# Kernel tuning notes

Hardware: AMD Instinct MI355X
Metric: run time of the kernel (lower is better)

Reference implementation:

```python
import jax, jax.numpy as jnp
import numpy as np
from jax import lax

DN = ('NCHW', 'OIHW', 'NCHW')

def conv2d(x, k):
    return lax.conv_general_dilated(x, k, (1, 1), 'SAME', dimension_numbers=DN)

def maxpool(x, k):
    # F.max_pool2d pads with -inf (stride 1, odd k -> SAME)
    return lax.reduce_window(x, jnp.array(-jnp.inf, x.dtype), lax.max,
                             (1, 1, k, k), (1, 1, 1, 1), 'SAME')

def avgpool(x, k):
    # F.avg_pool2d default count_include_pad=True -> sum with zero pad / k*k
    s = lax.reduce_window(x, jnp.array(0.0, x.dtype), lax.add,
                          (1, 1, k, k), (1, 1, 1, 1), 'SAME')
    return s / (k * k)

def erode(x, k):
    return -maxpool(-x, k)

def opening(x, k):
    return maxpool(erode(x, k), k)

def quantile(x, q):
    B = x.shape[0]
    return jnp.quantile(x.reshape(B, -1), q, axis=1).reshape(B, 1, 1, 1).astype(x.dtype)

_SOBEL_X = jnp.array([[-1, 0, 1], [-2, 0, 2], [-1, 0, 1]], jnp.float32).reshape(1, 1, 3, 3)
_SOBEL_Y = jnp.array([[1, 2, 1], [0, 0, 0], [-1, -2, -1]], jnp.float32).reshape(1, 1, 3, 3)

def sobelxy(x):
    return jnp.abs(conv2d(x, _SOBEL_X)) + jnp.abs(conv2d(x, _SOBEL_Y))

def _gauss_window(size=11, sigma=1.5):
    g = np.exp(-((np.arange(size) - size // 2) ** 2) / (2.0 * sigma ** 2))
    g = g / g.sum()
    return jnp.asarray(np.outer(g, g), jnp.float32).reshape(1, 1, size, size)

_SSIM_W = _gauss_window()

def ssim(x, y):
    # standard single-channel SSIM, gaussian 11x11 sigma=1.5, SAME padding
    C1, C2 = 0.01 ** 2, 0.03 ** 2
    mu1, mu2 = conv2d(x, _SSIM_W), conv2d(y, _SSIM_W)
    mu1_sq, mu2_sq, mu12 = mu1 * mu1, mu2 * mu2, mu1 * mu2
    s1 = conv2d(x * x, _SSIM_W) - mu1_sq
    s2 = conv2d(y * y, _SSIM_W) - mu2_sq
    s12 = conv2d(x * y, _SSIM_W) - mu12
    m = ((2 * mu12 + C1) * (2 * s12 + C2)) / ((mu1_sq + mu2_sq + C1) * (s1 + s2 + C2))
    return m.mean()

def compute_saliency(ir1):
    # multi-scale morphological top-hat, max over scales, mean-normalized
    sals = [ir1 - opening(ir1, k) for k in (9, 15, 31)]
    sal = jnp.maximum(jnp.maximum(sals[0], sals[1]), sals[2])
    return sal / (sal.mean(axis=(2, 3), keepdims=True) + 1e-6)

def halo_mask_builder(ir1, vis1):
    # surrogate for undefined PhysicsConsistentHaloMask: halo ring around IR highlights
    bright = (ir1 > quantile(ir1, 0.97)).astype(ir1.dtype)
    dilated = maxpool(bright, 15)
    return jnp.clip(dilated - bright, 0.0, 1.0)

_NEAR_RADIUS = 50
_c = np.arange(-_NEAR_RADIUS, _NEAR_RADIUS + 1)
_yy, _xx = np.meshgrid(_c, _c, indexing='ij')
_DISK = jnp.asarray((( _xx * _xx + _yy * _yy) <= _NEAR_RADIUS * _NEAR_RADIUS).astype(np.float32)).reshape(1, 1, 2 * _NEAR_RADIUS + 1, 2 * _NEAR_RADIUS + 1)

def build_distance_decay(M_light):
    near = conv2d((M_light > 0).astype(M_light.dtype), _DISK)
    return (near > 0).astype(M_light.dtype)


def setup_inputs() -> dict:
    key = jax.random.key(0)
    kA, kB, kF = jax.random.split(key, 3)
    shp = (4, 1, 512, 512)
    return {
        'image_A': jax.random.uniform(kA, shp, jnp.float32),
        'image_B': jax.random.uniform(kB, shp, jnp.float32),
        'image_fused': jax.random.uniform(kF, shp, jnp.float32),
    }


def reference(image_A, image_B, image_fused):
    w_l1, w_grad, w_ssim = 15.0, 14.0, 20.0
    lambda_halo, lambda_bloom = 0.3, 0.6
    blur_ks = 9

    ir1 = image_A[:, :1]
    vis1 = image_B[:, :1]
    fused1 = image_fused[:, :1]

    sal = compute_saliency(ir1)
    # get_M_mask: top_ratio_m=0.1, slope=20
    M = jax.nn.sigmoid(20.0 * (sal - quantile(sal, 0.9)))
    # get_M_light_mask
    M_light = ((sal > quantile(sal, 0.97)) & (ir1 > quantile(ir1, 0.97))).astype(sal.dtype)
    M_light = M_light * (vis1 > quantile(vis1, 0.97)).astype(sal.dtype)
    M = lax.stop_gradient(M)
    M_light = lax.stop_gradient(M_light)

    imax = jnp.maximum(image_A, image_B)
    imin = jnp.minimum(image_A, image_B)
    thr_ir = jnp.clip(quantile(image_A, 0.7), 0.45, 0.85)
    thr_vis = jnp.clip(quantile(image_B, 0.4), 0.3, 0.7)
    thr_vis_super = jnp.clip(quantile(image_B, 0.85), 0.75, 0.98)
    ir_bright = image_A > thr_ir
    vis_bright = image_B > thr_vis
    vis_super = image_B > thr_vis_super
    salient = jnp.where(vis_bright, imin, imax)
    salient = jnp.where(vis_super & ir_bright, imax, salient)
    intensity_target = M * salient + (1.0 - M) * imax

    loss_l1 = w_l1 * jnp.abs(image_fused - intensity_target).mean()

    gA, gB, gF = sobelxy(ir1), sobelxy(vis1), sobelxy(fused1)
    loss_grad = w_grad * jnp.abs(gF - jnp.maximum(gA, gB)).mean()

    loss_ssim = w_ssim * (1.0 - (0.5 * ssim(image_A, image_fused)
                                 + 0.5 * ssim(image_B, image_fused)))

    ir_b = avgpool(ir1, blur_ks)
    vis_b = avgpool(vis1, blur_ks)
    fused_b = jnp.clip(avgpool(fused1, blur_ks), 0.0, 1.0)

    halo = halo_mask_builder(ir1, vis1)
    Mhalo = jnp.clip(halo - M_light, 0.0, 1.0) * build_distance_decay(M_light)
    Mhalo = lax.stop_gradient(Mhalo)

    sum_mhalo = jnp.maximum(Mhalo.sum() + 1e-6, 1.0)
    loss_halo = (Mhalo * jax.nn.relu(fused_b - ir_b)).sum() / sum_mhalo
    sum_m = jnp.maximum(M.sum() + 1e-6, 1.0)
    loss_bloom = (M * jax.nn.relu(fused_b - vis_b)).sum() / sum_m

    weighted_hb = lambda_halo * loss_halo + lambda_bloom * loss_bloom
    fusion_loss = loss_l1 + loss_grad + loss_ssim + weighted_hb
    return (fusion_loss, loss_grad, loss_l1, loss_ssim, weighted_hb)
```

## Files before the change

kernel.cpp:

```cpp
#include <hip/hip_runtime.h>
#include <cmath>

#define BATCH 4
#define HGT 512
#define WID 512
#define PIX (HGT*WID)
#define NPIX (BATCH*PIX)

constexpr size_t OFF_SAL   = 0;
constexpr size_t OFF_ML    = OFF_SAL  + (size_t)NPIX*4;
constexpr size_t OFF_HALO  = OFF_ML   + (size_t)NPIX;
constexpr size_t OFF_DECAY = OFF_HALO + (size_t)NPIX;
constexpr size_t OFF_CNT   = OFF_DECAY+ (size_t)NPIX;
constexpr size_t OFF_PTS   = OFF_CNT  + 64;
constexpr size_t OFF_H1    = OFF_PTS  + (size_t)NPIX*4;
constexpr size_t OFF_H2    = OFF_H1   + (size_t)3*BATCH*4096*4;
constexpr size_t OFF_H3    = OFF_H2   + (size_t)14*BATCH*1024*4;
constexpr size_t OFF_ST1   = OFF_H3   + (size_t)14*BATCH*1024*4;
constexpr size_t OFF_ST2   = OFF_ST1  + (size_t)BATCH*16*8;
constexpr size_t OFF_OST   = OFF_ST2  + (size_t)BATCH*16*8;
constexpr size_t OFF_SCAL  = OFF_OST  + (size_t)BATCH*16*4;
constexpr size_t OFF_SPART = OFF_SCAL + (size_t)BATCH*16*4;
constexpr size_t OFF_PG    = OFF_SPART+ 1024*4;
constexpr size_t OFF_PSA   = OFF_PG   + 1024*4;
constexpr size_t OFF_PSB   = OFF_PSA  + 1024*4;
constexpr size_t OFF_P5    = OFF_PSB  + 1024*4;

constexpr size_t QHIST_BYTES = (size_t)(3*BATCH*4096 + 14*BATCH*1024 + 14*BATCH*1024)*4;

#define S_THR_IR 0
#define S_THR_VIS 1
#define S_THR_SUP 2
#define S_Q97A 3
#define S_Q97B 4
#define S_Q90S 5
#define S_Q97S 6
#define S_KM 8

#define QH_BLOCKS 128

struct QRanks { int rank[14]; int arr[14]; int nr; };
struct GaussArg { float g[11]; };
struct FracArg { float fA70, fA97, fB40, fB85, fB97, fS90, fS97; };

__device__ __forceinline__ unsigned keymap(float x){
  unsigned u = __float_as_uint(x);
  return (u & 0x80000000u) ? ~u : (u | 0x80000000u);
}
__device__ __forceinline__ float invkey(unsigned k){
  unsigned bits = (k & 0x80000000u) ? (k ^ 0x80000000u) : ~k;
  return __uint_as_float(bits);
}

__device__ __forceinline__ float block_sum(float v, float* red16, int tid){
  for (int o = 32; o > 0; o >>= 1) v += __shfl_down(v, o);
  if ((tid & 63) == 0) red16[tid >> 6] = v;
  __syncthreads();
  float s = (tid < 16) ? red16[tid] : 0.f;
  if (tid < 64) for (int o = 8; o > 0; o >>= 1) s += __shfl_down(s, o);
  __syncthreads();
  return s;
}

template<int IS_MIN>
__device__ __forceinline__ void sweep31_8(const float* __restrict__ in, int base, int st, float o[8]){
  float a[38];
  #pragma unroll
  for (int j = 0; j < 38; ++j) a[j] = in[base + j*st];
  float core = a[7];
  #pragma unroll
  for (int j = 8; j <= 30; ++j) core = IS_MIN ? fminf(core, a[j]) : fmaxf(core, a[j]);
  float pref[7];
  pref[6] = a[6];
  #pragma unroll
  for (int k = 5; k >= 0; --k) pref[k] = IS_MIN ? fminf(a[k], pref[k+1]) : fmaxf(a[k], pref[k+1]);
  float suf[8];
  suf[1] = a[31];
  #pragma unroll
  for (int k = 2; k <= 7; ++k) suf[k] = IS_MIN ? fminf(suf[k-1], a[30+k]) : fmaxf(suf[k-1], a[30+k]);
  o[0] = IS_MIN ? fminf(pref[0], core) : fmaxf(pref[0], core);
  #pragma unroll
  for (int k = 1; k <= 6; ++k){
    float t = IS_MIN ? fminf(core, suf[k]) : fmaxf(core, suf[k]);
    o[k] = IS_MIN ? fminf(pref[k], t) : fmaxf(pref[k], t);
  }
  o[7] = IS_MIN ? fminf(core, suf[7]) : fmaxf(core, suf[7]);
}

#define RS 97
__global__ __launch_bounds__(1024, 4) void open_k(const float* __restrict__ A,
                                                  float* __restrict__ sal, float* __restrict__ spart){
  __shared__ float buf0[92*RS];
  __shared__ float buf1[92*RS];
  __shared__ float red16[16];
  int b = blockIdx.z;
  int y0 = blockIdx.y*32, x0 = blockIdx.x*32;
  int tid = threadIdx.y*32 + threadIdx.x;
  int ly = threadIdx.y, lx = threadIdx.x;
  const float* Ab = A + ((size_t)b << 18);

  for (int idx = tid; idx < 92*92; idx += 1024){
    int r = idx / 92, c = idx % 92;
    int gy = y0 + r - 30, gx = x0 + c - 30;
    float v = 3.4e38f;
    if (gy >= 0 && gy < HGT && gx >= 0 && gx < WID) v = Ab[(gy << 9) + gx];
    buf0[r*RS + c] = v;
  }
  __syncthreads();
  float centerA = buf0[(ly+30)*RS + lx+30];

  for (int task = tid; task < 92*8; task += 1024){
    int r = task >> 3, seg = task & 7;
    int start = seg*8 - ((seg == 7) ? 2 : 0);
    float o[8];
    sweep31_8<1>(buf0, r*RS + start, 1, o);
    #pragma unroll
    for (int k = 0; k < 8; ++k) buf1[r*RS + start + k] = o[k];
  }
  __syncthreads();
  for (int task = tid; task < 62*8; task += 1024){
    int x = task >> 3, seg = task & 7;
    int start = seg*8 - ((seg == 7) ? 2 : 0);
    float o[8];
    sweep31_8<1>(buf1, start*RS + x, RS, o);
    int gx = x0 + x - 15;
    bool xin = (gx >= 0 && gx < WID);
    #pragma unroll
    for (int k = 0; k < 8; ++k){
      int y = start + k;
      int gy = y0 + y - 15;
      bool in = xin && (gy >= 0) && (gy < HGT);
      buf0[y*RS + x] = in ? o[k] : -3.4e38f;
    }
  }
  __syncthreads();
  for (int task = tid; task < 62*4; task += 1024){
    int r = task >> 2, seg = task & 3;
    int start = seg*8;
    float o[8];
    sweep31_8<0>(buf0, r*RS + start, 1, o);
    #pragma unroll
    for (int k = 0; k < 8; ++k) buf1[r*RS + start + k] = o[k];
  }
  __syncthreads();
  for (int task = tid; task < 32*4; task += 1024){
    int x = task >> 2, seg = task & 3;
    int start = seg*8;
    float o[8];
    sweep31_8<0>(buf1, start*RS + x, RS, o);
    #pragma unroll
    for (int k = 0; k < 8; ++k) buf0[(start+k)*RS + x] = o[k];
  }
  __syncthreads();
  size_t g = ((size_t)b << 18) + ((size_t)(y0+ly) << 9) + (x0+lx);
  float sv = centerA - buf0[ly*RS + lx];
  sal[g] = sv;
  float tot = block_sum(sv, red16, tid);
  if (tid == 0) spart[b*256 + blockIdx.y*16 + blockIdx.x] = tot;
}

__global__ __launch_bounds__(256) void qh1_k(const float* __restrict__ X0, const float* __restrict__ X1,
                                             const float* __restrict__ X2, unsigned* __restrict__ h1){
  __shared__ unsigned hist[4096];
  int b = blockIdx.y, z = blockIdx.z;
  const float* p = (z == 0 ? X0 : (z == 1 ? X1 : X2)) + (size_t)b*PIX;
  for (int i = threadIdx.x; i < 4096; i += 256) hist[i] = 0;
  __syncthreads();
  for (int i = blockIdx.x*256 + threadIdx.x; i < PIX; i += QH_BLOCKS*256){
    unsigned k = keymap(p[i]);
    atomicAdd(&hist[k >> 20], 1u);
  }
  __syncthreads();
  unsigned* g = h1 + ((size_t)(z*BATCH + b))*4096;
  for (int i = threadIdx.x; i < 4096; i += 256){
    unsigned c = hist[i];
    if (c) atomicAdd(&g[i], c);
  }
}

__global__ __launch_bounds__(1024) void qs1_k(const unsigned* __restrict__ h1, QRanks ra,
                                              int2* __restrict__ st1){
  __shared__ unsigned csum[1024];
  int zb = blockIdx.x; int z = zb / BATCH, b = zb % BATCH;
  const unsigned* h = h1 + (size_t)zb*4096;
  int t = threadIdx.x, base = t*4;
  unsigned c4[4]; unsigned own = 0;
  for (int j = 0; j < 4; ++j){ c4[j] = h[base+j]; own += c4[j]; }
  csum[t] = own; __syncthreads();
  for (int o = 1; o < 1024; o <<= 1){
    unsigned v = (t >= o) ? csum[t-o] : 0u;
    __syncthreads();
    csum[t] += v;
    __syncthreads();
  }
  unsigned incl = csum[t], excl = incl - own;
  for (int r = 0; r < ra.nr; ++r){
    if (ra.arr[r] != z) continue;
    unsigned rank = (unsigned)ra.rank[r];
    if (rank >= excl && rank < incl){
      unsigned rem = rank - excl;
      for (int j = 0; j < 4; ++j){
        if (rem < c4[j]){ st1[b*16 + r] = make_int2(base + j, (int)rem); break; }
        rem -= c4[j];
      }
    }
  }
}

__global__ __launch_bounds__(256) void qh2_k(const float* __restrict__ X0, const float* __restrict__ X1,
                                             const float* __restrict__ X2,
                                             const int2* __restrict__ st1, QRanks ra,
                                             unsigned* __restrict__ h2){
  __shared__ unsigned hist[6*1024];
  int b = blockIdx.y, z = blockIdx.z;
  int rl[6]; unsigned bins[6]; int nr = 0;
  #pragma unroll
  for (int r = 0; r < 14; ++r){
    if (r < ra.nr && ra.arr[r] == z && nr < 6){
      rl[nr] = r; bins[nr] = (unsigned)st1[b*16 + r].x; ++nr;
    }
  }
  const float* p = (z == 0 ? X0 : (z == 1 ? X1 : X2)) + (size_t)b*PIX;
  for (int i = threadIdx.x; i < 6*1024; i += 256) hist[i] = 0;
  __syncthreads();
  for (int i = blockIdx.x*256 + threadIdx.x; i < PIX; i += QH_BLOCKS*256){
    unsigned k = keymap(p[i]);
    unsigned top = k >> 20, mid = (k >> 10) & 0x3FFu;
    #pragma unroll
    for (int q = 0; q < 6; ++q)
      if (q < nr && top == bins[q]) atomicAdd(&hist[q*1024 + mid], 1u);
  }
  __syncthreads();
  #pragma unroll
  for (int q = 0; q < 6; ++q){
    if (q >= nr) break;
    unsigned* g = h2 + ((size_t)(rl[q]*BATCH + b))*1024;
    for (int i = threadIdx.x; i < 1024; i += 256){
      unsigned c = hist[q*1024 + i];
      if (c) atomicAdd(&g[i], c);
    }
  }
}

__global__ __launch_bounds__(1024) void qs2_k(const unsigned* __restrict__ h2,
                                              const int2* __restrict__ st1,
                                              int2* __restrict__ st2){
  __shared__ unsigned csum[1024];
  int rb = blockIdx.x; int r = rb / BATCH, b = rb % BATCH;
  const unsigned* h = h2 + (size_t)rb*1024;
  int t = threadIdx.x;
  unsigned own = h[t];
  csum[t] = own; __syncthreads();
  for (int o = 1; o < 1024; o <<= 1){
    unsigned v = (t >= o) ? csum[t-o] : 0u;
    __syncthreads();
    csum[t] += v;
    __syncthreads();
  }
  unsigned rank = (unsigned)st1[b*16 + r].y;
  unsigned incl = csum[t], excl = incl - own;
  if (rank >= excl && rank < incl) st2[b*16 + r] = make_int2(t, (int)(rank - excl));
}

__global__ __launch_bounds__(256) void qh3_k(const float* __restrict__ X0, const float* __restrict__ X1,
                                             const float* __restrict__ X2,
                                             const int2* __restrict__ st1, const int2* __restrict__ st2,
                                             QRanks ra, unsigned* __restrict__ h3){
  __shared__ unsigned hist[6*1024];
  int b = blockIdx.y, z = blockIdx.z;
  int rl[6]; unsigned key22[6]; int nr = 0;
  #pragma unroll
  for (int r = 0; r < 14; ++r){
    if (r < ra.nr && ra.arr[r] == z && nr < 6){
      rl[nr] = r;
      key22[nr] = (((unsigned)st1[b*16 + r].x) << 10) | (unsigned)st2[b*16 + r].x;
      ++nr;
    }
  }
  const float* p = (z == 0 ? X0 : (z == 1 ? X1 : X2)) + (size_t)b*PIX;
  for (int i = threadIdx.x; i < 6*1024; i += 256) hist[i] = 0;
  __syncthreads();
  for (int i = blockIdx.x*256 + threadIdx.x; i < PIX; i += QH_BLOCKS*256){
    unsigned k = keymap(p[i]);
    unsigned top22 = k >> 10, low = k & 0x3FFu;
    #pragma unroll
    for (int q = 0; q < 6; ++q)
      if (q < nr && top22 == key22[q]) atomicAdd(&hist[q*1024 + low], 1u);
  }
  __syncthreads();
  #pragma unroll
  for (int q = 0; q < 6; ++q){
    if (q >= nr) break;
    unsigned* g = h3 + ((size_t)(rl[q]*BATCH + b))*1024;
    for (int i = threadIdx.x; i < 1024; i += 256){
      unsigned c = hist[q*1024 + i];
      if (c) atomicAdd(&g[i], c);
    }
  }
}

__global__ __launch_bounds__(1024) void qs3_k(const unsigned* __restrict__ h3,
                                              const int2* __restrict__ st1, const int2* __restrict__ st2,
                                              float* __restrict__ ostat){
  __shared__ unsigned csum[1024];
  int rb = blockIdx.x; int r = rb / BATCH, b = rb % BATCH;
  const unsigned* h = h3 + (size_t)rb*1024;
  int t = threadIdx.x;
  unsigned own = h[t];
  csum[t] = own; __syncthreads();
  for (int o = 1; o < 1024; o <<= 1){
    unsigned v = (t >= o) ? csum[t-o] : 0u;
    __syncthreads();
    csum[t] += v;
    __syncthreads();
  }
  unsigned rank = (unsigned)st2[b*16 + r].y;
  unsigned incl = csum[t], excl = incl - own;
  if (rank >= excl && rank < incl){
    unsigned key = (((unsigned)st1[b*16 + r].x) << 20) | (((unsigned)st2[b*16 + r].x) << 10) | (unsigned)t;
    ostat[b*16 + r] = invkey(key);
  }
}

__global__ __launch_bounds__(1024) void finq_k(const float* __restrict__ spart,
                                               const float* __restrict__ ostat,
                                               float* __restrict__ scal, FracArg fr){
  __shared__ float red[1024];
  int t = threadIdx.x;
  red[t] = spart[t];
  __syncthreads();
  for (int o = 128; o > 0; o >>= 1){
    if ((t & 255) < o) red[t] += red[t + o];
    __syncthreads();
  }
  if (t < BATCH){
    int b = t;
    const float* o = ostat + b*16;
    float q70  = o[0]  + fr.fA70*(o[1]-o[0]);
    float q97a = o[2]  + fr.fA97*(o[3]-o[2]);
    float q40  = o[4]  + fr.fB40*(o[5]-o[4]);
    float q85  = o[6]  + fr.fB85*(o[7]-o[6]);
    float q97b = o[8]  + fr.fB97*(o[9]-o[8]);
    float q90s = o[10] + fr.fS90*(o[11]-o[10]);
    float q97s = o[12] + fr.fS97*(o[13]-o[12]);
    float c = red[b*256]*(1.0f/(float)PIX) + 1e-6f;
    scal[b*16 + S_THR_IR]  = fminf(fmaxf(q70, 0.45f), 0.85f);
    scal[b*16 + S_Q97A]    = q97a;
    scal[b*16 + S_THR_VIS] = fminf(fmaxf(q40, 0.3f),  0.7f);
    scal[b*16 + S_THR_SUP] = fminf(fmaxf(q85, 0.75f), 0.98f);
    scal[b*16 + S_Q97B]    = q97b;
    scal[b*16 + S_Q90S]    = q90s;
    scal[b*16 + S_Q97S]    = q97s;
    scal[b*16 + S_KM]      = 20.0f / c;
  }
}

__global__ __launch_bounds__(1024) void brighthalo_k(const float* __restrict__ A,
                                                     const float* __restrict__ Bv,
                                                     const float* __restrict__ sal,
                                                     const float* __restrict__ scal,
                                                     unsigned char* __restrict__ halo,
                                                     unsigned char* __restrict__ ml,
                                                     int* __restrict__ cnt, int* __restrict__ pts){
  constexpr int R = 7, TW = 32 + 2*R;
  __shared__ float bt[TW*TW];
  __shared__ float dX[TW*32];
  int b = blockIdx.z;
  float thrA = scal[b*16 + S_Q97A];
  float q97s = scal[b*16 + S_Q97S];
  float q97b = scal[b*16 + S_Q97B];
  int y0 = blockIdx.y*32, x0 = blockIdx.x*32;
  int tid = threadIdx.y*32 + threadIdx.x;
  const float* Ab = A + ((size_t)b << 18);
  for (int idx = tid; idx < TW*TW; idx += 1024){
    int ly = idx / TW, lx = idx % TW;
    int gy = y0 + ly - R, gx = x0 + lx - R;
    float v = 0.f;
    if (gy >= 0 && gy < HGT && gx >= 0 && gx < WID) v = (Ab[(gy << 9) + gx] > thrA) ? 1.f : 0.f;
    bt[idx] = v;
  }
  __syncthreads();
  for (int idx = tid; idx < TW*32; idx += 1024){
    int row = idx >> 5, c = idx & 31;
    float m = 0.f;
    #pragma unroll
    for (int j = 0; j <= 2*R; ++j) m = fmaxf(m, bt[row*TW + c + j]);
    dX[idx] = m;
  }
  __syncthreads();
  int ly = threadIdx.y, lx = threadIdx.x;
  float m = 0.f;
  #pragma unroll
  for (int j = 0; j <= 2*R; ++j) m = fmaxf(m, dX[(ly+j)*32 + lx]);
  bool brightc = bt[(ly+R)*TW + lx + R] > 0.5f;
  size_t g = ((size_t)b << 18) + ((size_t)(y0+ly) << 9) + (x0+lx);
  halo[g] = (m > 0.5f && !brightc) ? 1 : 0;
  bool mlv = brightc && (sal[g] > q97s) && (Bv[g] > q97b);
  ml[g] = mlv ? 1 : 0;
  if (mlv){
    int idx = atomicAdd(&cnt[b], 1);
    pts[((size_t)b << 18) + idx] = (int)(g & (PIX-1));
  }
}

__global__ __launch_bounds__(128) void paint_k(const int* __restrict__ cnt, const int* __restrict__ pts,
                                               unsigned char* __restrict__ decay){
  int b = blockIdx.y;
  int n = cnt[b];
  for (int p = blockIdx.x; p < n; p += gridDim.x){
    int rem = pts[((size_t)b << 18) + p];
    int y = rem >> 9, x = rem & (WID-1);
    int t = threadIdx.x;
    if (t < 101){
      int dy = t - 50;
      int yy = y + dy;
      if (yy >= 0 && yy < HGT){
        int d2 = 2500 - dy*dy;
        int wd = (int)sqrtf((float)d2);
        while ((wd+1)*(wd+1) <= d2) ++wd;
        while (wd*wd > d2) --wd;
        int xl = x - wd; if (xl < 0) xl = 0;
        int xr = x + wd; if (xr > WID-1) xr = WID-1;
        unsigned char* row = decay + ((size_t)b << 18) + (yy << 9);
        int xx = xl;
        while (xx <= xr && (xx & 3)) row[xx++] = 1;
        for (; xx + 3 <= xr; xx += 4) *(unsigned*)(row + xx) = 0x01010101u;
        for (; xx <= xr; ++xx) row[xx] = 1;
      }
    }
  }
}

__device__ __forceinline__ float sobel42(const float* t, int ly, int lx){
  float gx = (t[(ly-1)*42+lx+1] - t[(ly-1)*42+lx-1]) + 2.f*(t[ly*42+lx+1] - t[ly*42+lx-1])
           + (t[(ly+1)*42+lx+1] - t[(ly+1)*42+lx-1]);
  float gy = (t[(ly-1)*42+lx-1] + 2.f*t[(ly-1)*42+lx] + t[(ly-1)*42+lx+1])
           - (t[(ly+1)*42+lx-1] + 2.f*t[(ly+1)*42+lx] + t[(ly+1)*42+lx+1]);
  return fabsf(gx) + fabsf(gy);
}

__global__ __launch_bounds__(1024) void gradssim_k(const float* __restrict__ A, const float* __restrict__ Bv,
                                                   const float* __restrict__ F,
                                                   float* __restrict__ pg,
                                                   float* __restrict__ psa, float* __restrict__ psb,
                                                   GaussArg gw){
  __shared__ float ta[42*42], tb[42*42], tf[42*42];
  __shared__ float pl[5*1344];
  __shared__ float red16[16];
  int b = blockIdx.z;
  int y0 = blockIdx.y*32, x0 = blockIdx.x*32;
  int tid = threadIdx.y*32 + threadIdx.x;
  size_t ib = (size_t)b*PIX;
  for (int idx = tid; idx < 42*42; idx += 1024){
    int ly = idx/42, lx = idx%42;
    int gy = y0 + ly - 5, gx = x0 + lx - 5;
    float av = 0.f, bv = 0.f, fv = 0.f;
    if (gy >= 0 && gy < HGT && gx >= 0 && gx < WID){
      size_t g = ib + (size_t)gy*WID + gx;
      av = A[g]; bv = Bv[g]; fv = F[g];
    }
    ta[idx] = av; tb[idx] = bv; tf[idx] = fv;
  }
  __syncthreads();
  int ly = threadIdx.y, lx = threadIdx.x;
  int blk = (blockIdx.z*gridDim.y + blockIdx.y)*gridDim.x + blockIdx.x;

  float ga = sobel42(ta, ly+5, lx+5), gb = sobel42(tb, ly+5, lx+5), gf = sobel42(tf, ly+5, lx+5);
  float gval = fabsf(gf - fmaxf(ga, gb));
  float gs = block_sum(gval, red16, tid);
  if (tid == 0) pg[blk] = gs;

  float* hx  = pl + 0*1344; float* hxx = pl + 1*1344; float* hxf = pl + 2*1344;
  float* hf  = pl + 3*1344; float* hff = pl + 4*1344;
  for (int idx = tid; idx < 42*32; idx += 1024){
    int row = idx >> 5, col = idx & 31;
    float sf=0.f, sff=0.f;
    for (int j = 0; j < 11; ++j){
      float g = gw.g[j];
      float fv = tf[row*42 + col + j];
      sf += g*fv; sff += g*fv*fv;
    }
    hf[idx]=sf; hff[idx]=sff;
  }
  const float C1 = 1e-4f, C2 = 9e-4f;
  #pragma unroll
  for (int pass = 0; pass < 2; ++pass){
    const float* tx = pass ? tb : ta;
    for (int idx = tid; idx < 42*32; idx += 1024){
      int row = idx >> 5, col = idx & 31;
      float sx=0.f, sxx=0.f, sxf=0.f;
      for (int j = 0; j < 11; ++j){
        float g = gw.g[j];
        float xv = tx[row*42 + col + j], fv = tf[row*42 + col + j];
        sx += g*xv; sxx += g*xv*xv; sxf += g*xv*fv;
      }
      hx[idx]=sx; hxx[idx]=sxx; hxf[idx]=sxf;
    }
    __syncthreads();
    float mu1=0.f, mu2=0.f, cxx=0.f, cff=0.f, cxf=0.f;
    for (int j = 0; j < 11; ++j){
      float g = gw.g[j];
      int o = (ly+j)*32 + lx;
      mu1 += g*hx[o]; mu2 += g*hf[o];
      cxx += g*hxx[o]; cff += g*hff[o]; cxf += g*hxf[o];
    }
    float m11 = mu1*mu1, m22 = mu2*mu2, m12 = mu1*mu2;
    float s1 = cxx - m11, s2 = cff - m22, s12 = cxf - m12;
    float m = ((2.f*m12 + C1)*(2.f*s12 + C2)) / ((m11 + m22 + C1)*(s1 + s2 + C2));
    __syncthreads();
    float s = block_sum(m, red16, tid);
    if (tid == 0){ if (pass) psb[blk] = s; else psa[blk] = s; }
  }
}

__global__ __launch_bounds__(1024) void hb_k(const float* __restrict__ A, const float* __restrict__ Bv,
                                             const float* __restrict__ F, const float* __restrict__ sal,
                                             const float* __restrict__ scal,
                                             const unsigned char* __restrict__ ml,
                                             const unsigned char* __restrict__ halo,
                                             const unsigned char* __restrict__ decay,
                                             float* __restrict__ p5){
  __shared__ float ti[40*40], tv[40*40], tf[40*40];
  __shared__ float hi_[40*32], hv_[40*32], hf_[40*32];
  __shared__ float red16[16];
  int b = blockIdx.z;
  int y0 = blockIdx.y*32, x0 = blockIdx.x*32;
  int tid = threadIdx.y*32 + threadIdx.x;
  size_t ib = (size_t)b*PIX;
  for (int idx = tid; idx < 40*40; idx += 1024){
    int ly = idx/40, lx = idx%40;
    int gy = y0 + ly - 4, gx = x0 + lx - 4;
    float a = 0.f, v = 0.f, f = 0.f;
    if (gy >= 0 && gy < HGT && gx >= 0 && gx < WID){
      size_t g = ib + (size_t)gy*WID + gx;
      a = A[g]; v = Bv[g]; f = F[g];
    }
    ti[idx] = a; tv[idx] = v; tf[idx] = f;
  }
  __syncthreads();
  for (int idx = tid; idx < 40*32; idx += 1024){
    int row = idx >> 5, col = idx & 31;
    float si=0.f, sv=0.f, sf=0.f;
    for (int j = 0; j < 9; ++j){
      int o = row*40 + col + j;
      si += ti[o]; sv += tv[o]; sf += tf[o];
    }
    hi_[idx]=si; hv_[idx]=sv; hf_[idx]=sf;
  }
  __syncthreads();
  int ly = threadIdx.y, lx = threadIdx.x;
  float si=0.f, sv=0.f, sf=0.f;
  for (int j = 0; j < 9; ++j){
    int o = (ly+j)*32 + lx;
    si += hi_[o]; sv += hv_[o]; sf += hf_[o];
  }
  const float inv81 = 1.f/81.f;
  float ib_ = si*inv81, vb_ = sv*inv81;
  float fb_ = fminf(fmaxf(sf*inv81, 0.f), 1.f);
  size_t g = ib + ((size_t)(y0+ly) << 9) + (x0+lx);
  float q90s = scal[b*16 + S_Q90S], kM = scal[b*16 + S_KM];
  float M = 1.f/(1.f + expf(-kM*(sal[g] - q90s)));
  float mh = (halo[g] && !ml[g] && decay[g]) ? 1.f : 0.f;
  float v1 = mh*fmaxf(fb_ - ib_, 0.f);
  float v3 = M*fmaxf(fb_ - vb_, 0.f);
  float a = ti[(ly+4)*40 + lx+4], v = tv[(ly+4)*40 + lx+4], f = tf[(ly+4)*40 + lx+4];
  float imx = fmaxf(a, v), imn = fminf(a, v);
  bool irb = a > scal[b*16 + S_THR_IR];
  bool visb = v > scal[b*16 + S_THR_VIS];
  bool viss = v > scal[b*16 + S_THR_SUP];
  float salient = visb ? imn : imx;
  if (viss && irb) salient = imx;
  float target = M*salient + (1.f - M)*imx;
  float l1v = fabsf(f - target);

  float vals[5] = {v1, mh, v3, M, l1v};
  int blk = (blockIdx.z*gridDim.y + blockIdx.y)*gridDim.x + blockIdx.x;
  #pragma unroll
  for (int q = 0; q < 5; ++q){
    float s = block_sum(vals[q], red16, tid);
    if (tid == 0) p5[blk*5+q] = s;
  }
}

__global__ __launch_bounds__(1024) void final_k(const float* __restrict__ pg,
                                                const float* __restrict__ psa, const float* __restrict__ psb,
                                                const float* __restrict__ p5, float* __restrict__ out){
  __shared__ float red16[16];
  int t = threadIdx.x;
  float sumG = block_sum(pg[t], red16, t);
  float sA   = block_sum(psa[t], red16, t);
  float sB   = block_sum(psb[t], red16, t);
  float s5[5];
  #pragma unroll
  for (int q = 0; q < 5; ++q) s5[q] = block_sum(p5[t*5+q], red16, t);
  if (t == 0){
    const float inv = 1.f/(float)NPIX;
    float loss_grad = 14.f*sumG*inv;
    float loss_ssim = 20.f*(1.f - 0.5f*sA*inv - 0.5f*sB*inv);
    float lh = s5[0] / fmaxf(s5[1] + 1e-6f, 1.f);
    float lb = s5[2] / fmaxf(s5[3] + 1e-6f, 1.f);
    float whb = 0.3f*lh + 0.6f*lb;
    float loss_l1 = 15.f*s5[4]*inv;
    out[0] = loss_l1 + loss_grad + loss_ssim + whb;
    out[1] = loss_grad;
    out[2] = loss_l1;
    out[3] = loss_ssim;
    out[4] = whb;
  }
}

extern "C" void kernel_launch(void* const* d_in, const int* in_sizes, int n_in,
                              void* d_out, int out_size, void* d_ws, size_t ws_size,
                              hipStream_t stream) {
  const float* A  = (const float*)d_in[0];
  const float* Bv = (const float*)d_in[1];
  const float* F  = (const float*)d_in[2];
  float* out = (float*)d_out;
  char* w = (char*)d_ws;

  float* sal = (float*)(w + OFF_SAL);
  unsigned char* ml    = (unsigned char*)(w + OFF_ML);
  unsigned char* halo  = (unsigned char*)(w + OFF_HALO);
  unsigned char* decay = (unsigned char*)(w + OFF_DECAY);
  int* cnt = (int*)(w + OFF_CNT);
  int* pts = (int*)(w + OFF_PTS);
  unsigned* h1 = (unsigned*)(w + OFF_H1);
  unsigned* h2 = (unsigned*)(w + OFF_H2);
  unsigned* h3 = (unsigned*)(w + OFF_H3);
  int2* st1 = (int2*)(w + OFF_ST1);
  int2* st2 = (int2*)(w + OFF_ST2);
  float* ost  = (float*)(w + OFF_OST);
  float* scal = (float*)(w + OFF_SCAL);
  float* spart= (float*)(w + OFF_SPART);
  float* pg  = (float*)(w + OFF_PG);
  float* psa = (float*)(w + OFF_PSA);
  float* psb = (float*)(w + OFF_PSB);
  float* p5  = (float*)(w + OFF_P5);

  dim3 b256(256);
  dim3 gt(WID/32, HGT/32, BATCH), bt(32, 32);

  auto mkrank = [](double q, int* k0, double* fr){
    double pos = q*(double)(PIX-1);
    double fl = floor(pos);
    *k0 = (int)fl; *fr = pos - fl;
  };
  int kA70, kA97, kB40, kB85, kB97, kS90, kS97;
  double fA70, fA97, fB40, fB85, fB97, fS90, fS97;
  mkrank(0.70, &kA70, &fA70); mkrank(0.97, &kA97, &fA97);
  mkrank(0.40, &kB40, &fB40); mkrank(0.85, &kB85, &fB85); mkrank(0.97, &kB97, &fB97);
  mkrank(0.90, &kS90, &fS90); mkrank(0.97, &kS97, &fS97);

  hipMemsetAsync(w + OFF_H1, 0, QHIST_BYTES, stream);
  hipMemsetAsync(w + OFF_DECAY, 0, (size_t)NPIX + 64, stream);

  open_k<<<gt, bt, 0, stream>>>(A, sal, spart);

  QRanks ra{};
  {
    int rr[14] = {kA70, kA70+1, kA97, kA97+1,
                  kB40, kB40+1, kB85, kB85+1, kB97, kB97+1,
                  kS90, kS90+1, kS97, kS97+1};
    int aa[14] = {0,0,0,0, 1,1,1,1,1,1, 2,2,2,2};
    for (int i = 0; i < 14; ++i){ ra.rank[i]=rr[i]; ra.arr[i]=aa[i]; }
    ra.nr = 14;
  }
  qh1_k<<<dim3(QH_BLOCKS, BATCH, 3), b256, 0, stream>>>(A, Bv, sal, h1);
  qs1_k<<<3*BATCH, 1024, 0, stream>>>(h1, ra, st1);
  qh2_k<<<dim3(QH_BLOCKS, BATCH, 3), b256, 0, stream>>>(A, Bv, sal, st1, ra, h2);
  qs2_k<<<14*BATCH, 1024, 0, stream>>>(h2, st1, st2);
  qh3_k<<<dim3(QH_BLOCKS, BATCH, 3), b256, 0, stream>>>(A, Bv, sal, st1, st2, ra, h3);
  qs3_k<<<14*BATCH, 1024, 0, stream>>>(h3, st1, st2, ost);
  FracArg fr{(float)fA70, (float)fA97, (float)fB40, (float)fB85, (float)fB97, (float)fS90, (float)fS97};
  finq_k<<<1, 1024, 0, stream>>>(spart, ost, scal, fr);

  brighthalo_k<<<gt, bt, 0, stream>>>(A, Bv, sal, scal, halo, ml, cnt, pts);
  paint_k<<<dim3(256, BATCH), 128, 0, stream>>>(cnt, pts, decay);

  GaussArg ga{};
  {
    double g[11], s = 0.0;
    for (int i = 0; i < 11; ++i){ double d = (double)(i-5); g[i] = exp(-(d*d)/4.5); s += g[i]; }
    for (int i = 0; i < 11; ++i) ga.g[i] = (float)(g[i]/s);
  }
  gradssim_k<<<gt, bt, 0, stream>>>(A, Bv, F, pg, psa, psb, ga);
  hb_k<<<gt, bt, 0, stream>>>(A, Bv, F, sal, scal, ml, halo, decay, p5);

  final_k<<<1, 1024, 0, stream>>>(pg, psa, psb, p5, out);
}
```

Measured before the change: 153.0 us.

## Merge memsets, use wave-shuffle scans, vectorize histograms, fuse loss kernels

The workspace is reordered so one memset clears the decay, count and histogram regions together instead of two separate memsets. The three prefix-scan kernels replace a 1024-step shared-memory Hillis-Steele scan with a two-level wave shuffle scan. The three histogram passes read float4 instead of scalar floats. The gradient/SSIM and halo/bloom kernels are merged into one launch that splits work by blockIdx.z, which removes a launch at the cost of larger shared-memory use per block.

```diff
diff --git a/kernel.cpp b/kernel.cpp
--- a/kernel.cpp
+++ b/kernel.cpp
@@ -12,11 +12,13 @@
 constexpr size_t OFF_HALO  = OFF_ML   + (size_t)NPIX;
 constexpr size_t OFF_DECAY = OFF_HALO + (size_t)NPIX;
 constexpr size_t OFF_CNT   = OFF_DECAY+ (size_t)NPIX;
-constexpr size_t OFF_PTS   = OFF_CNT  + 64;
-constexpr size_t OFF_H1    = OFF_PTS  + (size_t)NPIX*4;
+constexpr size_t OFF_H1    = OFF_CNT  + 64;
 constexpr size_t OFF_H2    = OFF_H1   + (size_t)3*BATCH*4096*4;
 constexpr size_t OFF_H3    = OFF_H2   + (size_t)14*BATCH*1024*4;
-constexpr size_t OFF_ST1   = OFF_H3   + (size_t)14*BATCH*1024*4;
+constexpr size_t OFF_ZEND  = OFF_H3   + (size_t)14*BATCH*1024*4;
+constexpr size_t ZERO_BYTES= OFF_ZEND - OFF_DECAY;
+constexpr size_t OFF_PTS   = OFF_ZEND;
+constexpr size_t OFF_ST1   = OFF_PTS  + (size_t)NPIX*4;
 constexpr size_t OFF_ST2   = OFF_ST1  + (size_t)BATCH*16*8;
 constexpr size_t OFF_OST   = OFF_ST2  + (size_t)BATCH*16*8;
 constexpr size_t OFF_SCAL  = OFF_OST  + (size_t)BATCH*16*4;
@@ -26,8 +28,6 @@
 constexpr size_t OFF_PSB   = OFF_PSA  + 1024*4;
 constexpr size_t OFF_P5    = OFF_PSB  + 1024*4;
 
-constexpr size_t QHIST_BYTES = (size_t)(3*BATCH*4096 + 14*BATCH*1024 + 14*BATCH*1024)*4;
-
 #define S_THR_IR 0
 #define S_THR_VIS 1
 #define S_THR_SUP 2
@@ -60,6 +60,30 @@
   if (tid < 64) for (int o = 8; o > 0; o >>= 1) s += __shfl_down(s, o);
   __syncthreads();
   return s;
+}
+
+__device__ __forceinline__ unsigned block_scan_incl(unsigned own, unsigned* warpsum, int tid){
+  unsigned v = own;
+  int lane = tid & 63;
+  #pragma unroll
+  for (int o = 1; o < 64; o <<= 1){
+    unsigned t = __shfl_up(v, o, 64);
+    if (lane >= o) v += t;
+  }
+  if (lane == 63) warpsum[tid >> 6] = v;
+  __syncthreads();
+  if (tid < 16){
+    unsigned w = warpsum[tid];
+    #pragma unroll
+    for (int o = 1; o < 16; o <<= 1){
+      unsigned t = __shfl_up(w, o, 64);
+      if (tid >= o) w += t;
+    }
+    warpsum[tid] = w;
+  }
+  __syncthreads();
+  unsigned off = (tid >> 6) ? warpsum[(tid >> 6) - 1] : 0u;
+  return v + off;
 }
 
 template<int IS_MIN>
@@ -164,11 +188,15 @@
   __shared__ unsigned hist[4096];
   int b = blockIdx.y, z = blockIdx.z;
   const float* p = (z == 0 ? X0 : (z == 1 ? X1 : X2)) + (size_t)b*PIX;
+  const float4* p4 = (const float4*)p;
   for (int i = threadIdx.x; i < 4096; i += 256) hist[i] = 0;
   __syncthreads();
-  for (int i = blockIdx.x*256 + threadIdx.x; i < PIX; i += QH_BLOCKS*256){
-    unsigned k = keymap(p[i]);
-    atomicAdd(&hist[k >> 20], 1u);
+  for (int i = blockIdx.x*256 + threadIdx.x; i < PIX/4; i += QH_BLOCKS*256){
+    float4 v = p4[i];
+    atomicAdd(&hist[keymap(v.x) >> 20], 1u);
+    atomicAdd(&hist[keymap(v.y) >> 20], 1u);
+    atomicAdd(&hist[keymap(v.z) >> 20], 1u);
+    atomicAdd(&hist[keymap(v.w) >> 20], 1u);
   }
   __syncthreads();
   unsigned* g = h1 + ((size_t)(z*BATCH + b))*4096;
@@ -180,20 +208,14 @@
 
 __global__ __launch_bounds__(1024) void qs1_k(const unsigned* __restrict__ h1, QRanks ra,
                                               int2* __restrict__ st1){
-  __shared__ unsigned csum[1024];
+  __shared__ unsigned warpsum[16];
   int zb = blockIdx.x; int z = zb / BATCH, b = zb % BATCH;
   const unsigned* h = h1 + (size_t)zb*4096;
   int t = threadIdx.x, base = t*4;
   unsigned c4[4]; unsigned own = 0;
   for (int j = 0; j < 4; ++j){ c4[j] = h[base+j]; own += c4[j]; }
-  csum[t] = own; __syncthreads();
-  for (int o = 1; o < 1024; o <<= 1){
-    unsigned v = (t >= o) ? csum[t-o] : 0u;
-    __syncthreads();
-    csum[t] += v;
-    __syncthreads();
-  }
-  unsigned incl = csum[t], excl = incl - own;
+  unsigned incl = block_scan_incl(own, warpsum, t);
+  unsigned excl = incl - own;
   for (int r = 0; r < ra.nr; ++r){
     if (ra.arr[r] != z) continue;
     unsigned rank = (unsigned)ra.rank[r];
@@ -221,14 +243,20 @@
     }
   }
   const float* p = (z == 0 ? X0 : (z == 1 ? X1 : X2)) + (size_t)b*PIX;
+  const float4* p4 = (const float4*)p;
   for (int i = threadIdx.x; i < 6*1024; i += 256) hist[i] = 0;
   __syncthreads();
-  for (int i = blockIdx.x*256 + threadIdx.x; i < PIX; i += QH_BLOCKS*256){
-    unsigned k = keymap(p[i]);
-    unsigned top = k >> 20, mid = (k >> 10) & 0x3FFu;
-    #pragma unroll
-    for (int q = 0; q < 6; ++q)
-      if (q < nr && top == bins[q]) atomicAdd(&hist[q*1024 + mid], 1u);
+  for (int i = blockIdx.x*256 + threadIdx.x; i < PIX/4; i += QH_BLOCKS*256){
+    float4 v = p4[i];
+    float e[4] = {v.x, v.y, v.z, v.w};
+    #pragma unroll
+    for (int j = 0; j < 4; ++j){
+      unsigned k = keymap(e[j]);
+      unsigned top = k >> 20, mid = (k >> 10) & 0x3FFu;
+      #pragma unroll
+      for (int q = 0; q < 6; ++q)
+        if (q < nr && top == bins[q]) atomicAdd(&hist[q*1024 + mid], 1u);
+    }
   }
   __syncthreads();
   #pragma unroll
@@ -245,20 +273,14 @@
 __global__ __launch_bounds__(1024) void qs2_k(const unsigned* __restrict__ h2,
                                               const int2* __restrict__ st1,
                                               int2* __restrict__ st2){
-  __shared__ unsigned csum[1024];
+  __shared__ unsigned warpsum[16];
   int rb = blockIdx.x; int r = rb / BATCH, b = rb % BATCH;
   const unsigned* h = h2 + (size_t)rb*1024;
   int t = threadIdx.x;
   unsigned own = h[t];
-  csum[t] = own; __syncthreads();
-  for (int o = 1; o < 1024; o <<= 1){
-    unsigned v = (t >= o) ? csum[t-o] : 0u;
-    __syncthreads();
-    csum[t] += v;
-    __syncthreads();
-  }
+  unsigned incl = block_scan_incl(own, warpsum, t);
+  unsigned excl = incl - own;
   unsigned rank = (unsigned)st1[b*16 + r].y;
-  unsigned incl = csum[t], excl = incl - own;
   if (rank >= excl && rank < incl) st2[b*16 + r] = make_int2(t, (int)(rank - excl));
 }
 
@@ -278,14 +300,20 @@
     }
   }
   const float* p = (z == 0 ? X0 : (z == 1 ? X1 : X2)) + (size_t)b*PIX;
+  const float4* p4 = (const float4*)p;
   for (int i = threadIdx.x; i < 6*1024; i += 256) hist[i] = 0;
   __syncthreads();
-  for (int i = blockIdx.x*256 + threadIdx.x; i < PIX; i += QH_BLOCKS*256){
-    unsigned k = keymap(p[i]);
-    unsigned top22 = k >> 10, low = k & 0x3FFu;
-    #pragma unroll
-    for (int q = 0; q < 6; ++q)
-      if (q < nr && top22 == key22[q]) atomicAdd(&hist[q*1024 + low], 1u);
+  for (int i = blockIdx.x*256 + threadIdx.x; i < PIX/4; i += QH_BLOCKS*256){
+    float4 v = p4[i];
+    float e[4] = {v.x, v.y, v.z, v.w};
+    #pragma unroll
+    for (int j = 0; j < 4; ++j){
+      unsigned k = keymap(e[j]);
+      unsigned top22 = k >> 10, low = k & 0x3FFu;
+      #pragma unroll
+      for (int q = 0; q < 6; ++q)
+        if (q < nr && top22 == key22[q]) atomicAdd(&hist[q*1024 + low], 1u);
+    }
   }
   __syncthreads();
   #pragma unroll
@@ -302,20 +330,14 @@
 __global__ __launch_bounds__(1024) void qs3_k(const unsigned* __restrict__ h3,
                                               const int2* __restrict__ st1, const int2* __restrict__ st2,
                                               float* __restrict__ ostat){
-  __shared__ unsigned csum[1024];
+  __shared__ unsigned warpsum[16];
   int rb = blockIdx.x; int r = rb / BATCH, b = rb % BATCH;
   const unsigned* h = h3 + (size_t)rb*1024;
   int t = threadIdx.x;
   unsigned own = h[t];
-  csum[t] = own; __syncthreads();
-  for (int o = 1; o < 1024; o <<= 1){
-    unsigned v = (t >= o) ? csum[t-o] : 0u;
-    __syncthreads();
-    csum[t] += v;
-    __syncthreads();
-  }
+  unsigned incl = block_scan_incl(own, warpsum, t);
+  unsigned excl = incl - own;
   unsigned rank = (unsigned)st2[b*16 + r].y;
-  unsigned incl = csum[t], excl = incl - own;
   if (rank >= excl && rank < incl){
     unsigned key = (((unsigned)st1[b*16 + r].x) << 20) | (((unsigned)st2[b*16 + r].x) << 10) | (unsigned)t;
     ostat[b*16 + r] = invkey(key);
@@ -439,146 +461,143 @@
   return fabsf(gx) + fabsf(gy);
 }
 
-__global__ __launch_bounds__(1024) void gradssim_k(const float* __restrict__ A, const float* __restrict__ Bv,
-                                                   const float* __restrict__ F,
-                                                   float* __restrict__ pg,
-                                                   float* __restrict__ psa, float* __restrict__ psb,
-                                                   GaussArg gw){
-  __shared__ float ta[42*42], tb[42*42], tf[42*42];
-  __shared__ float pl[5*1344];
+__global__ __launch_bounds__(1024) void losses_k(const float* __restrict__ A, const float* __restrict__ Bv,
+                                                 const float* __restrict__ F, const float* __restrict__ sal,
+                                                 const float* __restrict__ scal,
+                                                 const unsigned char* __restrict__ ml,
+                                                 const unsigned char* __restrict__ halo,
+                                                 const unsigned char* __restrict__ decay,
+                                                 float* __restrict__ pg,
+                                                 float* __restrict__ psa, float* __restrict__ psb,
+                                                 float* __restrict__ p5, GaussArg gw){
+  __shared__ float smem[12012];
   __shared__ float red16[16];
-  int b = blockIdx.z;
+  int zz = blockIdx.z;
   int y0 = blockIdx.y*32, x0 = blockIdx.x*32;
   int tid = threadIdx.y*32 + threadIdx.x;
-  size_t ib = (size_t)b*PIX;
-  for (int idx = tid; idx < 42*42; idx += 1024){
-    int ly = idx/42, lx = idx%42;
-    int gy = y0 + ly - 5, gx = x0 + lx - 5;
-    float av = 0.f, bv = 0.f, fv = 0.f;
-    if (gy >= 0 && gy < HGT && gx >= 0 && gx < WID){
-      size_t g = ib + (size_t)gy*WID + gx;
-      av = A[g]; bv = Bv[g]; fv = F[g];
-    }
-    ta[idx] = av; tb[idx] = bv; tf[idx] = fv;
-  }
-  __syncthreads();
   int ly = threadIdx.y, lx = threadIdx.x;
-  int blk = (blockIdx.z*gridDim.y + blockIdx.y)*gridDim.x + blockIdx.x;
-
-  float ga = sobel42(ta, ly+5, lx+5), gb = sobel42(tb, ly+5, lx+5), gf = sobel42(tf, ly+5, lx+5);
-  float gval = fabsf(gf - fmaxf(ga, gb));
-  float gs = block_sum(gval, red16, tid);
-  if (tid == 0) pg[blk] = gs;
-
-  float* hx  = pl + 0*1344; float* hxx = pl + 1*1344; float* hxf = pl + 2*1344;
-  float* hf  = pl + 3*1344; float* hff = pl + 4*1344;
-  for (int idx = tid; idx < 42*32; idx += 1024){
-    int row = idx >> 5, col = idx & 31;
-    float sf=0.f, sff=0.f;
-    for (int j = 0; j < 11; ++j){
-      float g = gw.g[j];
-      float fv = tf[row*42 + col + j];
-      sf += g*fv; sff += g*fv*fv;
-    }
-    hf[idx]=sf; hff[idx]=sff;
-  }
-  const float C1 = 1e-4f, C2 = 9e-4f;
-  #pragma unroll
-  for (int pass = 0; pass < 2; ++pass){
-    const float* tx = pass ? tb : ta;
+
+  if (zz < BATCH){
+    int b = zz;
+    size_t ib = (size_t)b*PIX;
+    float* ta = smem; float* tb = smem + 1764; float* tf = smem + 3528;
+    float* pl = smem + 5292;
+    for (int idx = tid; idx < 42*42; idx += 1024){
+      int r = idx/42, c = idx%42;
+      int gy = y0 + r - 5, gx = x0 + c - 5;
+      float av = 0.f, bv = 0.f, fv = 0.f;
+      if (gy >= 0 && gy < HGT && gx >= 0 && gx < WID){
+        size_t g = ib + (size_t)gy*WID + gx;
+        av = A[g]; bv = Bv[g]; fv = F[g];
+      }
+      ta[idx] = av; tb[idx] = bv; tf[idx] = fv;
+    }
+    __syncthreads();
+    int blk = (b*gridDim.y + blockIdx.y)*gridDim.x + blockIdx.x;
+
+    float ga = sobel42(ta, ly+5, lx+5), gb = sobel42(tb, ly+5, lx+5), gf = sobel42(tf, ly+5, lx+5);
+    float gval = fabsf(gf - fmaxf(ga, gb));
+    float gs = block_sum(gval, red16, tid);
+    if (tid == 0) pg[blk] = gs;
+
+    float* hx  = pl + 0*1344; float* hxx = pl + 1*1344; float* hxf = pl + 2*1344;
+    float* hf  = pl + 3*1344; float* hff = pl + 4*1344;
     for (int idx = tid; idx < 42*32; idx += 1024){
       int row = idx >> 5, col = idx & 31;
-      float sx=0.f, sxx=0.f, sxf=0.f;
+      float sf=0.f, sff=0.f;
       for (int j = 0; j < 11; ++j){
         float g = gw.g[j];
-        float xv = tx[row*42 + col + j], fv = tf[row*42 + col + j];
-        sx += g*xv; sxx += g*xv*xv; sxf += g*xv*fv;
+        float fv = tf[row*42 + col + j];
+        sf += g*fv; sff += g*fv*fv;
       }
-      hx[idx]=sx; hxx[idx]=sxx; hxf[idx]=sxf;
+      hf[idx]=sf; hff[idx]=sff;
+    }
+    const float C1 = 1e-4f, C2 = 9e-4f;
+    #pragma unroll
+    for (int pass = 0; pass < 2; ++pass){
+      const float* tx = pass ? tb : ta;
+      for (int idx = tid; idx < 42*32; idx += 1024){
+        int row = idx >> 5, col = idx & 31;
+        float sx=0.f, sxx=0.f, sxf=0.f;
+        for (int j = 0; j < 11; ++j){
+          float g = gw.g[j];
+          float xv = tx[row*42 + col + j], fv = tf[row*42 + col + j];
+          sx += g*xv; sxx += g*xv*xv; sxf += g*xv*fv;
+        }
+        hx[idx]=sx; hxx[idx]=sxx; hxf[idx]=sxf;
+      }
+      __syncthreads();
+      float mu1=0.f, mu2=0.f, cxx=0.f, cff=0.f, cxf=0.f;
+      for (int j = 0; j < 11; ++j){
+        float g = gw.g[j];
+        int o = (ly+j)*32 + lx;
+        mu1 += g*hx[o]; mu2 += g*hf[o];
+        cxx += g*hxx[o]; cff += g*hff[o]; cxf += g*hxf[o];
+      }
+      float m11 = mu1*mu1, m22 = mu2*mu2, m12 = mu1*mu2;
+      float s1 = cxx - m11, s2 = cff - m22, s12 = cxf - m12;
+      float m = ((2.f*m12 + C1)*(2.f*s12 + C2)) / ((m11 + m22 + C1)*(s1 + s2 + C2));
+      __syncthreads();
+      float s = block_sum(m, red16, tid);
+      if (tid == 0){ if (pass) psb[blk] = s; else psa[blk] = s; }
+    }
+  } else {
+    int b = zz - BATCH;
+    size_t ib = (size_t)b*PIX;
+    float* ti = smem; float* tv = smem + 1600; float* tf = smem + 3200;
+    float* hi_ = smem + 4800; float* hv_ = smem + 6080; float* hf_ = smem + 7360;
+    for (int idx = tid; idx < 40*40; idx += 1024){
+      int r = idx/40, c = idx%40;
+      int gy = y0 + r - 4, gx = x0 + c - 4;
+      float a = 0.f, v = 0.f, f = 0.f;
+      if (gy >= 0 && gy < HGT && gx >= 0 && gx < WID){
+        size_t g = ib + (size_t)gy*WID + gx;
+        a = A[g]; v = Bv[g]; f = F[g];
+      }
+      ti[idx] = a; tv[idx] = v; tf[idx] = f;
     }
     __syncthreads();
-    float mu1=0.f, mu2=0.f, cxx=0.f, cff=0.f, cxf=0.f;
-    for (int j = 0; j < 11; ++j){
-      float g = gw.g[j];
-      int o = (ly+j)*32 + lx;
-      mu1 += g*hx[o]; mu2 += g*hf[o];
-      cxx += g*hxx[o]; cff += g*hff[o]; cxf += g*hxf[o];
-    }
-    float m11 = mu1*mu1, m22 = mu2*mu2, m12 = mu1*mu2;
-    float s1 = cxx - m11, s2 = cff - m22, s12 = cxf - m12;
-    float m = ((2.f*m12 + C1)*(2.f*s12 + C2)) / ((m11 + m22 + C1)*(s1 + s2 + C2));
+    for (int idx = tid; idx < 40*32; idx += 1024){
+      int row = idx >> 5, col = idx & 31;
+      float si=0.f, sv=0.f, sf=0.f;
+      for (int j = 0; j < 9; ++j){
+        int o = row*40 + col + j;
+        si += ti[o]; sv += tv[o]; sf += tf[o];
+      }
+      hi_[idx]=si; hv_[idx]=sv; hf_[idx]=sf;
+    }
     __syncthreads();
-    float s = block_sum(m, red16, tid);
-    if (tid == 0){ if (pass) psb[blk] = s; else psa[blk] = s; }
-  }
-}
-
-__global__ __launch_bounds__(1024) void hb_k(const float* __restrict__ A, const float* __restrict__ Bv,
-                                             const float* __restrict__ F, const float* __restrict__ sal,
-                                             const float* __restrict__ scal,
-                                             const unsigned char* __restrict__ ml,
-                                             const unsigned char* __restrict__ halo,
-                                             const unsigned char* __restrict__ decay,
-                                             float* __restrict__ p5){
-  __shared__ float ti[40*40], tv[40*40], tf[40*40];
-  __shared__ float hi_[40*32], hv_[40*32], hf_[40*32];
-  __shared__ float red16[16];
-  int b = blockIdx.z;
-  int y0 = blockIdx.y*32, x0 = blockIdx.x*32;
-  int tid = threadIdx.y*32 + threadIdx.x;
-  size_t ib = (size_t)b*PIX;
-  for (int idx = tid; idx < 40*40; idx += 1024){
-    int ly = idx/40, lx = idx%40;
-    int gy = y0 + ly - 4, gx = x0 + lx - 4;
-    float a = 0.f, v = 0.f, f = 0.f;
-    if (gy >= 0 && gy < HGT && gx >= 0 && gx < WID){
-      size_t g = ib + (size_t)gy*WID + gx;
-      a = A[g]; v = Bv[g]; f = F[g];
-    }
-    ti[idx] = a; tv[idx] = v; tf[idx] = f;
-  }
-  __syncthreads();
-  for (int idx = tid; idx < 40*32; idx += 1024){
-    int row = idx >> 5, col = idx & 31;
     float si=0.f, sv=0.f, sf=0.f;
     for (int j = 0; j < 9; ++j){
-      int o = row*40 + col + j;
-      si += ti[o]; sv += tv[o]; sf += tf[o];
-    }
-    hi_[idx]=si; hv_[idx]=sv; hf_[idx]=sf;
-  }
-  __syncthreads();
-  int ly = threadIdx.y, lx = threadIdx.x;
-  float si=0.f, sv=0.f, sf=0.f;
-  for (int j = 0; j < 9; ++j){
-    int o = (ly+j)*32 + lx;
-    si += hi_[o]; sv += hv_[o]; sf += hf_[o];
-  }
-  const float inv81 = 1.f/81.f;
-  float ib_ = si*inv81, vb_ = sv*inv81;
-  float fb_ = fminf(fmaxf(sf*inv81, 0.f), 1.f);
-  size_t g = ib + ((size_t)(y0+ly) << 9) + (x0+lx);
-  float q90s = scal[b*16 + S_Q90S], kM = scal[b*16 + S_KM];
-  float M = 1.f/(1.f + expf(-kM*(sal[g] - q90s)));
-  float mh = (halo[g] && !ml[g] && decay[g]) ? 1.f : 0.f;
-  float v1 = mh*fmaxf(fb_ - ib_, 0.f);
-  float v3 = M*fmaxf(fb_ - vb_, 0.f);
-  float a = ti[(ly+4)*40 + lx+4], v = tv[(ly+4)*40 + lx+4], f = tf[(ly+4)*40 + lx+4];
-  float imx = fmaxf(a, v), imn = fminf(a, v);
-  bool irb = a > scal[b*16 + S_THR_IR];
-  bool visb = v > scal[b*16 + S_THR_VIS];
-  bool viss = v > scal[b*16 + S_THR_SUP];
-  float salient = visb ? imn : imx;
-  if (viss && irb) salient = imx;
-  float target = M*salient + (1.f - M)*imx;
-  float l1v = fabsf(f - target);
-
-  float vals[5] = {v1, mh, v3, M, l1v};
-  int blk = (blockIdx.z*gridDim.y + blockIdx.y)*gridDim.x + blockIdx.x;
-  #pragma unroll
-  for (int q = 0; q < 5; ++q){
-    float s = block_sum(vals[q], red16, tid);
-    if (tid == 0) p5[blk*5+q] = s;
+      int o = (ly+j)*32 + lx;
+      si += hi_[o]; sv += hv_[o]; sf += hf_[o];
+    }
+    const float inv81 = 1.f/81.f;
+    float ib_ = si*inv81, vb_ = sv*inv81;
+    float fb_ = fminf(fmaxf(sf*inv81, 0.f), 1.f);
+    size_t g = ib + ((size_t)(y0+ly) << 9) + (x0+lx);
+    float q90s = scal[b*16 + S_Q90S], kM = scal[b*16 + S_KM];
+    float M = 1.f/(1.f + expf(-kM*(sal[g] - q90s)));
+    float mh = (halo[g] && !ml[g] && decay[g]) ? 1.f : 0.f;
+    float v1 = mh*fmaxf(fb_ - ib_, 0.f);
+    float v3 = M*fmaxf(fb_ - vb_, 0.f);
+    float a = ti[(ly+4)*40 + lx+4], v = tv[(ly+4)*40 + lx+4], f = tf[(ly+4)*40 + lx+4];
+    float imx = fmaxf(a, v), imn = fminf(a, v);
+    bool irb = a > scal[b*16 + S_THR_IR];
+    bool visb = v > scal[b*16 + S_THR_VIS];
+    bool viss = v > scal[b*16 + S_THR_SUP];
+    float salient = visb ? imn : imx;
+    if (viss && irb) salient = imx;
+    float target = M*salient + (1.f - M)*imx;
+    float l1v = fabsf(f - target);
+
+    float vals[5] = {v1, mh, v3, M, l1v};
+    int blk = (b*gridDim.y + blockIdx.y)*gridDim.x + blockIdx.x;
+    #pragma unroll
+    for (int q = 0; q < 5; ++q){
+      float s = block_sum(vals[q], red16, tid);
+      if (tid == 0) p5[blk*5+q] = s;
+    }
   }
 }
 
@@ -651,8 +670,7 @@
   mkrank(0.40, &kB40, &fB40); mkrank(0.85, &kB85, &fB85); mkrank(0.97, &kB97, &fB97);
   mkrank(0.90, &kS90, &fS90); mkrank(0.97, &kS97, &fS97);
 
-  hipMemsetAsync(w + OFF_H1, 0, QHIST_BYTES, stream);
-  hipMemsetAsync(w + OFF_DECAY, 0, (size_t)NPIX + 64, stream);
+  hipMemsetAsync(w + OFF_DECAY, 0, ZERO_BYTES, stream);
 
   open_k<<<gt, bt, 0, stream>>>(A, sal, spart);
 
@@ -683,8 +701,8 @@
     for (int i = 0; i < 11; ++i){ double d = (double)(i-5); g[i] = exp(-(d*d)/4.5); s += g[i]; }
     for (int i = 0; i < 11; ++i) ga.g[i] = (float)(g[i]/s);
   }
-  gradssim_k<<<gt, bt, 0, stream>>>(A, Bv, F, pg, psa, psb, ga);
-  hb_k<<<gt, bt, 0, stream>>>(A, Bv, F, sal, scal, ml, halo, decay, p5);
+  losses_k<<<dim3(WID/32, HGT/32, 2*BATCH), bt, 0, stream>>>(A, Bv, F, sal, scal, ml, halo, decay,
+                                                             pg, psa, psb, p5, ga);
 
   final_k<<<1, 1024, 0, stream>>>(pg, psa, psb, p5, out);
 }
```

Result: faster. 143.8 us, median of 2 (-6.0%).
